# Kernel optimization log

Measured on AMD Instinct MI355X. Metric: run time of the kernel, lower is better.

Reference implementation:

```python
import jax, jax.numpy as jnp
import numpy as np

B, L, H = 8, 512, 768
W = 5          # max_phrase_len
K = 32         # max_phrases
P = 256        # phrase_dim
EPS = 1e-5
NEG = -1e30


def layernorm(x, g, b):
    m = jnp.mean(x, axis=-1, keepdims=True)
    v = jnp.var(x, axis=-1, keepdims=True)
    return (x - m) * jax.lax.rsqrt(v + EPS) * g + b


def setup_inputs() -> dict:
    key = jax.random.key(0)
    ks = jax.random.split(key, 12)
    s = 0.02
    return {
        "hidden": jax.random.normal(ks[0], (B, L, H), dtype=jnp.float32),
        "attention_mask": jnp.ones((B, L), dtype=jnp.int32),
        # span_scorer: Linear(4H->H), LayerNorm(H), ReLU, Linear(H->1)
        "w1": jax.random.normal(ks[1], (4 * H, H), dtype=jnp.float32) * s,
        "b1": jnp.zeros((H,), dtype=jnp.float32),
        "g1": jnp.ones((H,), dtype=jnp.float32),
        "beta1": jnp.zeros((H,), dtype=jnp.float32),
        "w2": jax.random.normal(ks[2], (H, 1), dtype=jnp.float32) * s,
        "b2": jnp.zeros((1,), dtype=jnp.float32),
        # proj: Linear(H->P)
        "wp": jax.random.normal(ks[3], (H, P), dtype=jnp.float32) * s,
        "bp": jnp.zeros((P,), dtype=jnp.float32),
        # attention_gate: Linear(H->H/2), Tanh, Linear(H/2->1)
        "wg1": jax.random.normal(ks[4], (H, H // 2), dtype=jnp.float32) * s,
        "bg1": jnp.zeros((H // 2,), dtype=jnp.float32),
        "wg2": jax.random.normal(ks[5], (H // 2, 1), dtype=jnp.float32) * s,
        "bg2": jnp.zeros((1,), dtype=jnp.float32),
        # out_norm: LayerNorm(P)
        "gout": jnp.ones((P,), dtype=jnp.float32),
        "bout": jnp.zeros((P,), dtype=jnp.float32),
    }


def reference(hidden, attention_mask, w1, b1, g1, beta1, w2, b2,
              wp, bp, wg1, bg1, wg2, bg2, gout, bout):
    mask = attention_mask.astype(bool)  # [B,L]
    # validity of span (i, j=i+w): all tokens i..i+w in mask and i+w < L
    valids = []
    v = mask
    for w in range(W):
        if w > 0:
            shifted = jnp.pad(mask[:, w:], ((0, 0), (0, w)), constant_values=False)
            v = v & shifted
        valids.append(v)
    valid = jnp.stack(valids, axis=2)  # [B,L,W]

    # span means via prefix sums
    prefix = jnp.pad(jnp.cumsum(hidden, axis=1), ((0, 0), (1, 0), (0, 0)))  # [B,L+1,H]
    i_idx = jnp.arange(L)
    j_idx = jnp.minimum(i_idx[:, None] + jnp.arange(W)[None, :], L - 1)  # [L,W]

    start = hidden[:, :, None, :]                                  # [B,L,1,H]
    end = hidden[:, j_idx]                                         # [B,L,W,H]
    span_sum = prefix[:, j_idx + 1] - prefix[:, i_idx][:, :, None, :]
    mean = span_sum / (jnp.arange(W, dtype=hidden.dtype) + 1.0)[None, None, :, None]
    diff = end - start
    start_b = jnp.broadcast_to(start, end.shape)
    feat = jnp.concatenate([start_b, end, mean, diff], axis=-1)    # [B,L,W,4H]

    h = feat @ w1 + b1
    h = jax.nn.relu(layernorm(h, g1, beta1))                       # dropout is eval-mode identity
    score = (h @ w2 + b2)[..., 0]                                  # [B,L,W]
    score = jnp.where(valid, score, NEG)

    flat_scores = score.reshape(B, L * W)
    top_scores, top_idx = jax.lax.top_k(flat_scores, K)            # [B,K]
    phrase_masks = top_scores > NEG / 2

    mean_flat = mean.reshape(B, L * W, H)
    embs = jnp.take_along_axis(mean_flat, top_idx[..., None], axis=1)  # [B,K,H]
    embs = jnp.where(phrase_masks[..., None], embs, 0.0)               # zero-pad features
    phrase_scores = jnp.where(phrase_masks, top_scores, -10.0)

    ti = top_idx // W
    tw = top_idx % W
    spans = jnp.stack([ti, ti + tw], axis=-1)                      # [B,K,2]
    spans = jnp.where(phrase_masks[..., None], spans, 0)

    gate_logits = (jnp.tanh(embs @ wg1 + bg1) @ wg2 + bg2)[..., 0]  # [B,K]
    gate_logits = jnp.where(phrase_masks, gate_logits, -1e9)
    phrase_attention = jax.nn.softmax(gate_logits, axis=-1)

    phrase_embeds = layernorm(embs @ wp + bp, gout, bout)           # [B,K,P]
    return phrase_embeds, phrase_masks, phrase_attention, phrase_scores, spans
```

## Files before the change

### kernel.cpp

```cpp
#include <hip/hip_runtime.h>
#include <float.h>
#include <math.h>

#define B_   8
#define L_   512
#define H_   768
#define W_   5
#define K_   32
#define P_   256
#define EPS_ 1e-5f
#define NEG_ -1e30f

typedef _Float16 half8 __attribute__((ext_vector_type(8)));
typedef _Float16 half4v __attribute__((ext_vector_type(4)));
typedef float floatx4 __attribute__((ext_vector_type(4)));

static const size_t OFF_X   = 0;
static const size_t OFF_AH  = 9437184;
static const size_t OFF_AL  = 11010048;
static const size_t OFF_BH  = 12582912;
static const size_t OFF_BL  = 13467648;
static const size_t OFF_SC  = 14352384;
static const size_t OFF_TS  = 14372864;
static const size_t OFF_TI  = 14373120;
static const size_t OFF_GL  = 14373376;
static const size_t OFF_EMB = 14373632;
static const size_t OFF_Y   = 14570240;

#define A_SCALE 8.0f
#define B_SCALE 64.0f
#define INV_SCALE (1.0f / 512.0f)

__global__ __launch_bounds__(256) void prep_kernel(const float* __restrict__ hid,
                                                   const float* __restrict__ w1,
                                                   _Float16* __restrict__ ah,
                                                   _Float16* __restrict__ al,
                                                   _Float16* __restrict__ bh,
                                                   _Float16* __restrict__ bl) {
    __shared__ float ld[64][65];
    if (blockIdx.x < 3072) {
        int idx = (blockIdx.x * 256 + threadIdx.x) * 4;
        float4 x = *(const float4*)(hid + idx);
        float xs[4] = {x.x * A_SCALE, x.y * A_SCALE, x.z * A_SCALE, x.w * A_SCALE};
        half4v h, l;
#pragma unroll
        for (int i = 0; i < 4; ++i) {
            _Float16 hi = (_Float16)xs[i];
            h[i] = hi;
            l[i] = (_Float16)(xs[i] - (float)hi);
        }
        *(half4v*)(ah + idx) = h;
        *(half4v*)(al + idx) = l;
    } else {
        int bid = blockIdx.x - 3072;
        int n0 = (bid / 12) * 64;
        int k0 = (bid % 12) * 64;
        int t = threadIdx.x;
        int rsel = n0 / 768;
        int c0 = n0 - rsel * 768;
#pragma unroll 4
        for (int r = 0; r < 16; ++r) {
            int idx = r * 256 + t;
            int kk = idx >> 6, nn = idx & 63;
            int k = k0 + kk, c = c0 + nn;
            float v;
            if (rsel == 0)      v = w1[(size_t)k * 768 + c] - w1[(size_t)(2304 + k) * 768 + c];
            else if (rsel == 1) v = w1[(size_t)(768 + k) * 768 + c] + w1[(size_t)(2304 + k) * 768 + c];
            else                v = w1[(size_t)(1536 + k) * 768 + c];
            ld[kk][nn] = v * B_SCALE;
        }
        __syncthreads();
#pragma unroll 4
        for (int r = 0; r < 16; ++r) {
            int idx = r * 256 + t;
            int nn = idx >> 6, kk = idx & 63;
            float v = ld[kk][nn];
            _Float16 h = (_Float16)v;
            _Float16 lo = (_Float16)(v - (float)h);
            size_t o = (size_t)(n0 + nn) * 768 + k0 + kk;
            bh[o] = h;
            bl[o] = lo;
        }
    }
}

typedef const __attribute__((address_space(1))) void* gas_ptr;
typedef __attribute__((address_space(3))) void* las_ptr;
__device__ __forceinline__ void async_ld16(const _Float16* g, _Float16* l) {
    __builtin_amdgcn_global_load_lds((gas_ptr)g, (las_ptr)l, 16, 0, 0);
}

__global__ __launch_bounds__(256) void mfma_gemm_kernel(const _Float16* __restrict__ Ah,
                                                        const _Float16* __restrict__ Al,
                                                        const _Float16* __restrict__ Bh,
                                                        const _Float16* __restrict__ Bl,
                                                        float* __restrict__ C) {
    __shared__ _Float16 sAh[2 * 4096];
    __shared__ _Float16 sAl[2 * 4096];
    __shared__ _Float16 sBh[2 * 2048];
    __shared__ _Float16 sBl[2 * 2048];
    int tid = threadIdx.x;
    int lane = tid & 63;
    int wave = tid >> 6;
    int m0 = blockIdx.x * 128, n0 = blockIdx.y * 64;

    const _Float16* src = (wave == 0) ? Ah : (wave == 1) ? Al : (wave == 2) ? Bh : Bl;
    _Float16* dstb = (wave == 0) ? sAh : (wave == 1) ? sAl : (wave == 2) ? sBh : sBl;
    int psz  = (wave < 2) ? 4096 : 2048;
    int nch  = (wave < 2) ? 8 : 4;
    int row0 = (wave < 2) ? m0 : n0;
    int qg = (lane & 3) ^ ((lane >> 3) & 3);
    const _Float16* gp = src + (size_t)(row0 + (lane >> 2)) * 768 + qg * 8;

    int wr = wave >> 1, wc = wave & 1;
    int off_lane = (lane & 15) * 64 + (((lane >> 4) ^ ((lane >> 1) & 3)) * 16);
    floatx4 acc[4][2];
#pragma unroll
    for (int i = 0; i < 4; ++i)
#pragma unroll
        for (int j = 0; j < 2; ++j)
            acc[i][j] = (floatx4){0.f, 0.f, 0.f, 0.f};

#pragma unroll
    for (int c = 0; c < 8; ++c) {
        if (c < nch) async_ld16(gp + (size_t)c * 16 * 768, dstb + c * 512);
    }

    int parity = 0;
    for (int k0 = 0; k0 < 768; k0 += 32) {
        __syncthreads();
        if (k0 + 32 < 768) {
            _Float16* dst = dstb + (parity ^ 1) * psz;
            const _Float16* g = gp + k0 + 32;
#pragma unroll
            for (int c = 0; c < 8; ++c) {
                if (c < nch) async_ld16(g + (size_t)c * 16 * 768, dst + c * 512);
            }
        }

        const char* bAh = (const char*)sAh + parity * 8192 + wr * 4096 + off_lane;
        const char* bAl = (const char*)sAl + parity * 8192 + wr * 4096 + off_lane;
        const char* bBh = (const char*)sBh + parity * 4096 + wc * 2048 + off_lane;
        const char* bBl = (const char*)sBl + parity * 4096 + wc * 2048 + off_lane;
        half8 a_h[4], a_l[4], b_h[2], b_l[2];
#pragma unroll
        for (int i = 0; i < 4; ++i) {
            a_h[i] = *(const half8*)(bAh + i * 1024);
            a_l[i] = *(const half8*)(bAl + i * 1024);
        }
#pragma unroll
        for (int j = 0; j < 2; ++j) {
            b_h[j] = *(const half8*)(bBh + j * 1024);
            b_l[j] = *(const half8*)(bBl + j * 1024);
        }
#pragma unroll
        for (int i = 0; i < 4; ++i)
#pragma unroll
            for (int j = 0; j < 2; ++j) {
                acc[i][j] = __builtin_amdgcn_mfma_f32_16x16x32_f16(a_h[i], b_h[j], acc[i][j], 0, 0, 0);
                acc[i][j] = __builtin_amdgcn_mfma_f32_16x16x32_f16(a_h[i], b_l[j], acc[i][j], 0, 0, 0);
                acc[i][j] = __builtin_amdgcn_mfma_f32_16x16x32_f16(a_l[i], b_h[j], acc[i][j], 0, 0, 0);
            }
        parity ^= 1;
    }

    int colc = lane & 15, quad = lane >> 4;
#pragma unroll
    for (int i = 0; i < 4; ++i) {
#pragma unroll
        for (int r = 0; r < 4; ++r) {
            int row = m0 + wr * 64 + i * 16 + quad * 4 + r;
            float* Cp = C + (size_t)row * 2304 + n0 + wc * 32 + colc;
#pragma unroll
            for (int j = 0; j < 2; ++j)
                Cp[j * 16] = acc[i][j][r] * INV_SCALE;
        }
    }
}

__global__ __launch_bounds__(256) void score_kernel(const float* __restrict__ X,
                                                    const int* __restrict__ mask,
                                                    const float* __restrict__ b1,
                                                    const float* __restrict__ g1,
                                                    const float* __restrict__ beta1,
                                                    const float* __restrict__ w2,
                                                    const float* __restrict__ b2,
                                                    float* __restrict__ scores) {
    int wave = threadIdx.x >> 6;
    int lane = threadIdx.x & 63;
    int bi = blockIdx.x * 4 + wave;
    int b = bi >> 9, i = bi & 511;

    float4 a[3], b1c[3], g1c[3], btc[3], w2c[3], ss[3], e[3];
    const float4* Xrow = (const float4*)(X + (size_t)bi * 2304);
#pragma unroll
    for (int q = 0; q < 3; ++q) {
        int f = lane + q * 64;
        a[q]   = Xrow[f];
        b1c[q] = ((const float4*)b1)[f];
        g1c[q] = ((const float4*)g1)[f];
        btc[q] = ((const float4*)beta1)[f];
        w2c[q] = ((const float4*)w2)[f];
        ss[q]  = make_float4(0.f, 0.f, 0.f, 0.f);
    }
    float bias2 = b2[0];
    int jcur = i - 1;
    float sc_loc[W_];

    for (int w = 0; w < W_; ++w) {
        int j = min(i + w, 511);
        const float4* Xj = (const float4*)(X + (size_t)(b * 512 + j) * 2304);
        if (j > jcur) {
#pragma unroll
            for (int q = 0; q < 3; ++q) {
                int f = lane + q * 64;
                float4 cc = Xj[384 + f];
                ss[q].x += cc.x; ss[q].y += cc.y; ss[q].z += cc.z; ss[q].w += cc.w;
                e[q] = Xj[192 + f];
            }
            jcur = j;
        }
        float invw = 1.0f / (float)(w + 1);
        float4 h[3];
        float psum = 0.f;
#pragma unroll
        for (int q = 0; q < 3; ++q) {
            h[q].x = a[q].x + e[q].x + ss[q].x * invw + b1c[q].x;
            h[q].y = a[q].y + e[q].y + ss[q].y * invw + b1c[q].y;
            h[q].z = a[q].z + e[q].z + ss[q].z * invw + b1c[q].z;
            h[q].w = a[q].w + e[q].w + ss[q].w * invw + b1c[q].w;
            psum += h[q].x + h[q].y + h[q].z + h[q].w;
        }
#pragma unroll
        for (int m = 1; m < 64; m <<= 1) psum += __shfl_xor(psum, m, 64);
        float mean = psum * (1.f / 768.f);

        float pv = 0.f;
#pragma unroll
        for (int q = 0; q < 3; ++q) {
            float dx = h[q].x - mean, dy = h[q].y - mean, dz = h[q].z - mean, dw = h[q].w - mean;
            pv += dx * dx + dy * dy + dz * dz + dw * dw;
        }
#pragma unroll
        for (int m = 1; m < 64; m <<= 1) pv += __shfl_xor(pv, m, 64);
        float rstd = rsqrtf(pv * (1.f / 768.f) + EPS_);

        float pd = 0.f;
#pragma unroll
        for (int q = 0; q < 3; ++q) {
            float yx = fmaxf((h[q].x - mean) * rstd * g1c[q].x + btc[q].x, 0.f);
            float yy = fmaxf((h[q].y - mean) * rstd * g1c[q].y + btc[q].y, 0.f);
            float yz = fmaxf((h[q].z - mean) * rstd * g1c[q].z + btc[q].z, 0.f);
            float yw = fmaxf((h[q].w - mean) * rstd * g1c[q].w + btc[q].w, 0.f);
            pd += yx * w2c[q].x + yy * w2c[q].y + yz * w2c[q].z + yw * w2c[q].w;
        }
#pragma unroll
        for (int m = 1; m < 64; m <<= 1) pd += __shfl_xor(pd, m, 64);
        sc_loc[w] = pd + bias2;
    }

    if (lane < W_) {
        int w = lane;
        bool ok = (i + w) < 512;
        if (ok) {
            for (int t = 0; t <= w; ++t) ok = ok && (mask[b * 512 + i + t] != 0);
        }
        scores[b * 2560 + i * 5 + w] = ok ? sc_loc[w] : NEG_;
    }
}

__global__ __launch_bounds__(256) void topk_kernel(const float* __restrict__ scores,
                                                   float* __restrict__ tops,
                                                   int* __restrict__ topi,
                                                   float* __restrict__ out_masks,
                                                   float* __restrict__ out_scores,
                                                   float* __restrict__ out_spans) {
    int b = blockIdx.x;
    int tid = threadIdx.x;
    int lane = tid & 63;
    int wv = tid >> 6;
    __shared__ float sc[2560];
    __shared__ float wv_v[4];
    __shared__ int   wv_i[4];
    for (int t = tid; t < 2560; t += 256) sc[t] = scores[b * 2560 + t];
    __syncthreads();

    for (int k = 0; k < K_; ++k) {
        float bv = -FLT_MAX; int bix = 1 << 30;
        for (int t = tid; t < 2560; t += 256) {
            float v = sc[t];
            if (v > bv || (v == bv && t < bix)) { bv = v; bix = t; }
        }
#pragma unroll
        for (int m = 1; m < 64; m <<= 1) {
            float v2 = __shfl_xor(bv, m, 64);
            int   i2 = __shfl_xor(bix, m, 64);
            if (v2 > bv || (v2 == bv && i2 < bix)) { bv = v2; bix = i2; }
        }
        if (lane == 0) { wv_v[wv] = bv; wv_i[wv] = bix; }
        __syncthreads();
        if (tid == 0) {
            float tv = wv_v[0]; int tix = wv_i[0];
            for (int q = 1; q < 4; ++q) {
                if (wv_v[q] > tv || (wv_v[q] == tv && wv_i[q] < tix)) { tv = wv_v[q]; tix = wv_i[q]; }
            }
            tops[b * 32 + k] = tv;
            topi[b * 32 + k] = tix;
            bool m = tv > (NEG_ * 0.5f);
            out_masks[b * 32 + k] = m ? 1.0f : 0.0f;
            out_scores[b * 32 + k] = m ? tv : -10.0f;
            int tI = tix / 5, tw = tix % 5;
            out_spans[(b * 32 + k) * 2 + 0] = m ? (float)tI : 0.0f;
            out_spans[(b * 32 + k) * 2 + 1] = m ? (float)(tI + tw) : 0.0f;
            sc[tix] = -FLT_MAX;
        }
        __syncthreads();
    }
}

__global__ __launch_bounds__(256) void gather_emb_kernel(const float* __restrict__ hidden,
                                                         const float* __restrict__ tops,
                                                         const int* __restrict__ topi,
                                                         float* __restrict__ Embs) {
    int bk = blockIdx.x;
    int b = bk >> 5;
    int tid = threadIdx.x;
    int idx = topi[bk];
    bool valid = tops[bk] > (NEG_ * 0.5f);
    int tI = idx / 5, tw = idx % 5;
    int jend = min(tI + tw, L_ - 1);
    float inv = 1.0f / (float)(tw + 1);
#pragma unroll
    for (int q = 0; q < 3; ++q) {
        int c = tid + q * 256;
        float s = 0.f;
        if (valid) {
            for (int l = tI; l <= jend; ++l) s += hidden[(size_t)(b * 512 + l) * 768 + c];
            s *= inv;
        }
        Embs[(size_t)bk * 768 + c] = s;
    }
}

__global__ __launch_bounds__(256) void phrase_gemm_kernel(const float* __restrict__ Embs,
                                                          const float* __restrict__ wg1,
                                                          const float* __restrict__ bg1,
                                                          const float* __restrict__ wp,
                                                          const float* __restrict__ bp,
                                                          float* __restrict__ Y) {
    __shared__ float As[32][34];
    __shared__ float Bs[32][64];
    int tid = threadIdx.x;
    int m0 = blockIdx.x * 32;
    int cn0 = blockIdx.y * 64;
    const float* Wp; const float* biasp; int ldw;
    if (cn0 < 384) { Wp = wg1 + cn0;        biasp = bg1 + cn0;        ldw = 384; }
    else           { Wp = wp + (cn0 - 384); biasp = bp + (cn0 - 384); ldw = 256; }

    int tx = tid & 15;
    int ty = tid >> 4;
    int ar = tid >> 3, akq = (tid & 7) * 4;
    int bk = tid >> 3, bcq = (tid & 7) * 8;
    float acc[2][4] = {};

    for (int k0 = 0; k0 < 768; k0 += 32) {
        float4 av  = *(const float4*)(Embs + (size_t)(m0 + ar) * 768 + k0 + akq);
        float4 bv0 = *(const float4*)(Wp + (size_t)(k0 + bk) * ldw + bcq);
        float4 bv1 = *(const float4*)(Wp + (size_t)(k0 + bk) * ldw + bcq + 4);
        __syncthreads();
        As[akq + 0][ar] = av.x;
        As[akq + 1][ar] = av.y;
        As[akq + 2][ar] = av.z;
        As[akq + 3][ar] = av.w;
        *(float4*)&Bs[bk][bcq]     = bv0;
        *(float4*)&Bs[bk][bcq + 4] = bv1;
        __syncthreads();
#pragma unroll
        for (int kk = 0; kk < 32; ++kk) {
            float2 a = *(const float2*)&As[kk][ty * 2];
            float4 b = *(const float4*)&Bs[kk][tx * 4];
            acc[0][0] += a.x * b.x; acc[0][1] += a.x * b.y; acc[0][2] += a.x * b.z; acc[0][3] += a.x * b.w;
            acc[1][0] += a.y * b.x; acc[1][1] += a.y * b.y; acc[1][2] += a.y * b.z; acc[1][3] += a.y * b.w;
        }
    }
#pragma unroll
    for (int i = 0; i < 2; ++i) {
        float* Yp = Y + (size_t)(m0 + ty * 2 + i) * 640 + cn0 + tx * 4;
        float4 o = make_float4(acc[i][0] + biasp[tx * 4 + 0], acc[i][1] + biasp[tx * 4 + 1],
                               acc[i][2] + biasp[tx * 4 + 2], acc[i][3] + biasp[tx * 4 + 3]);
        *(float4*)Yp = o;
    }
}

__global__ __launch_bounds__(256) void phrase_post_kernel(const float* __restrict__ Y,
                                                          const float* __restrict__ wg2,
                                                          const float* __restrict__ bg2,
                                                          const float* __restrict__ tops,
                                                          const float* __restrict__ gout,
                                                          const float* __restrict__ bout,
                                                          float* __restrict__ gate,
                                                          float* __restrict__ out_embeds) {
    int wv = threadIdx.x >> 6, lane = threadIdx.x & 63;
    int row = blockIdx.x * 4 + wv;
    const float* Yrow = Y + (size_t)row * 640;

    float s = 0.f;
#pragma unroll
    for (int q = 0; q < 6; ++q) {
        int c = lane + q * 64;
        s += tanhf(Yrow[c]) * wg2[c];
    }
#pragma unroll
    for (int m = 1; m < 64; m <<= 1) s += __shfl_xor(s, m, 64);
    if (lane == 0) {
        bool valid = tops[row] > (NEG_ * 0.5f);
        gate[row] = valid ? (s + bg2[0]) : -1e9f;
    }

    float4 p = *(const float4*)(Yrow + 384 + lane * 4);
    float sm = p.x + p.y + p.z + p.w;
#pragma unroll
    for (int m = 1; m < 64; m <<= 1) sm += __shfl_xor(sm, m, 64);
    float mean = sm * (1.f / 256.f);
    float dx = p.x - mean, dy = p.y - mean, dz = p.z - mean, dw = p.w - mean;
    float v = dx * dx + dy * dy + dz * dz + dw * dw;
#pragma unroll
    for (int m = 1; m < 64; m <<= 1) v += __shfl_xor(v, m, 64);
    float rstd = rsqrtf(v * (1.f / 256.f) + EPS_);
    int c = lane * 4;
    float4 o;
    o.x = dx * rstd * gout[c]     + bout[c];
    o.y = dy * rstd * gout[c + 1] + bout[c + 1];
    o.z = dz * rstd * gout[c + 2] + bout[c + 2];
    o.w = dw * rstd * gout[c + 3] + bout[c + 3];
    *(float4*)(out_embeds + (size_t)row * 256 + c) = o;
}

__global__ void attn_kernel(const float* __restrict__ gate, float* __restrict__ out_attn) {
    int b = threadIdx.x;
    if (b < 8) {
        float mx = -FLT_MAX;
        for (int k = 0; k < 32; ++k) mx = fmaxf(mx, gate[b * 32 + k]);
        float e[32];
        float s = 0.f;
        for (int k = 0; k < 32; ++k) { e[k] = expf(gate[b * 32 + k] - mx); s += e[k]; }
        float inv = 1.f / s;
        for (int k = 0; k < 32; ++k) out_attn[b * 32 + k] = e[k] * inv;
    }
}

extern "C" void kernel_launch(void* const* d_in, const int* in_sizes, int n_in,
                              void* d_out, int out_size, void* d_ws, size_t ws_size,
                              hipStream_t stream) {
    const float* hidden = (const float*)d_in[0];
    const int*   amask  = (const int*)d_in[1];
    const float* w1     = (const float*)d_in[2];
    const float* b1     = (const float*)d_in[3];
    const float* g1     = (const float*)d_in[4];
    const float* beta1  = (const float*)d_in[5];
    const float* w2     = (const float*)d_in[6];
    const float* b2     = (const float*)d_in[7];
    const float* wp     = (const float*)d_in[8];
    const float* bp     = (const float*)d_in[9];
    const float* wg1    = (const float*)d_in[10];
    const float* bg1    = (const float*)d_in[11];
    const float* wg2    = (const float*)d_in[12];
    const float* bg2    = (const float*)d_in[13];
    const float* gout   = (const float*)d_in[14];
    const float* bout   = (const float*)d_in[15];

    float* ws = (float*)d_ws;
    float*     X    = ws + OFF_X;
    _Float16*  ah   = (_Float16*)(ws + OFF_AH);
    _Float16*  al   = (_Float16*)(ws + OFF_AL);
    _Float16*  bh   = (_Float16*)(ws + OFF_BH);
    _Float16*  bl   = (_Float16*)(ws + OFF_BL);
    float*     sc   = ws + OFF_SC;
    float*     ts   = ws + OFF_TS;
    int*       ti   = (int*)(ws + OFF_TI);
    float*     gl   = ws + OFF_GL;
    float*     Embs = ws + OFF_EMB;
    float*     Y    = ws + OFF_Y;

    float* out = (float*)d_out;
    float* out_embeds = out;
    float* out_masks  = out + 65536;
    float* out_attn   = out + 65792;
    float* out_scores = out + 66048;
    float* out_spans  = out + 66304;

    prep_kernel<<<3504, 256, 0, stream>>>(hidden, w1, ah, al, bh, bl);
    mfma_gemm_kernel<<<dim3(32, 36), 256, 0, stream>>>(ah, al, bh, bl, X);
    score_kernel<<<1024, 256, 0, stream>>>(X, amask, b1, g1, beta1, w2, b2, sc);
    topk_kernel<<<8, 256, 0, stream>>>(sc, ts, ti, out_masks, out_scores, out_spans);
    gather_emb_kernel<<<256, 256, 0, stream>>>(hidden, ts, ti, Embs);
    phrase_gemm_kernel<<<dim3(8, 10), 256, 0, stream>>>(Embs, wg1, bg1, wp, bp, Y);
    phrase_post_kernel<<<64, 256, 0, stream>>>(Y, wg2, bg2, ts, gout, bout, gl, out_embeds);
    attn_kernel<<<1, 64, 0, stream>>>(gl, out_attn);
}
```

Before: 276.3 us.

## Rewrite top-k as per-thread sorted lists with packed 64-bit key reduction

Each thread loads its 10 scores and packs each one into a 64-bit key: an order-preserving float encoding in the high bits and an inverted index in the low bits. The thread sorts its keys locally with an odd-even transposition network and keeps only its head key live. Each of the 32 selection rounds then does a single packed max reduction, and only the winning thread advances to its next key. This removes the 10-element shared-memory rescan per round and the separate index comparison. The cost is more register pressure for the sort and two 32-bit shuffles per reduction step.

```diff
diff --git a/kernel.cpp b/kernel.cpp
--- a/kernel.cpp
+++ b/kernel.cpp
@@ -1,6 +1,7 @@
 #include <hip/hip_runtime.h>
 #include <float.h>
 #include <math.h>
+#include <stdint.h>
 
 #define B_   8
 #define L_   512
@@ -269,6 +270,13 @@
     }
 }
 
+__device__ __forceinline__ uint64_t shfl_xor_u64(uint64_t x, int m) {
+    uint32_t lo = (uint32_t)x, hi = (uint32_t)(x >> 32);
+    lo = (uint32_t)__shfl_xor((int)lo, m, 64);
+    hi = (uint32_t)__shfl_xor((int)hi, m, 64);
+    return ((uint64_t)hi << 32) | lo;
+}
+
 __global__ __launch_bounds__(256) void topk_kernel(const float* __restrict__ scores,
                                                    float* __restrict__ tops,
                                                    int* __restrict__ topi,
@@ -279,42 +287,68 @@
     int tid = threadIdx.x;
     int lane = tid & 63;
     int wv = tid >> 6;
-    __shared__ float sc[2560];
-    __shared__ float wv_v[4];
-    __shared__ int   wv_i[4];
-    for (int t = tid; t < 2560; t += 256) sc[t] = scores[b * 2560 + t];
-    __syncthreads();
+    __shared__ uint64_t lists[256 * 9];
+    __shared__ uint64_t wmax[4];
+    __shared__ uint64_t gS;
+
+    uint64_t v[10];
+#pragma unroll
+    for (int q = 0; q < 10; ++q) {
+        int t = q * 256 + tid;
+        float f = scores[b * 2560 + t];
+        uint32_t bits = __float_as_uint(f);
+        uint32_t mk = bits ^ ((bits & 0x80000000u) ? 0xFFFFFFFFu : 0x80000000u);
+        v[q] = ((uint64_t)mk << 32) | (uint64_t)(0xFFFFFFFFu - (uint32_t)t);
+    }
+#pragma unroll
+    for (int p = 0; p < 5; ++p) {
+#pragma unroll
+        for (int i = 0; i < 9; i += 2) {
+            if (v[i] < v[i + 1]) { uint64_t t = v[i]; v[i] = v[i + 1]; v[i + 1] = t; }
+        }
+#pragma unroll
+        for (int i = 1; i < 9; i += 2) {
+            if (v[i] < v[i + 1]) { uint64_t t = v[i]; v[i] = v[i + 1]; v[i + 1] = t; }
+        }
+    }
+#pragma unroll
+    for (int j = 0; j < 9; ++j) lists[tid * 9 + j] = v[j + 1];
+    uint64_t my = v[0];
+    int h = 0;
 
     for (int k = 0; k < K_; ++k) {
-        float bv = -FLT_MAX; int bix = 1 << 30;
-        for (int t = tid; t < 2560; t += 256) {
-            float v = sc[t];
-            if (v > bv || (v == bv && t < bix)) { bv = v; bix = t; }
-        }
-#pragma unroll
-        for (int m = 1; m < 64; m <<= 1) {
-            float v2 = __shfl_xor(bv, m, 64);
-            int   i2 = __shfl_xor(bix, m, 64);
-            if (v2 > bv || (v2 == bv && i2 < bix)) { bv = v2; bix = i2; }
-        }
-        if (lane == 0) { wv_v[wv] = bv; wv_i[wv] = bix; }
+        uint64_t m = my;
+#pragma unroll
+        for (int s = 1; s < 64; s <<= 1) {
+            uint64_t o = shfl_xor_u64(m, s);
+            if (o > m) m = o;
+        }
+        if (lane == 0) wmax[wv] = m;
         __syncthreads();
         if (tid == 0) {
-            float tv = wv_v[0]; int tix = wv_i[0];
-            for (int q = 1; q < 4; ++q) {
-                if (wv_v[q] > tv || (wv_v[q] == tv && wv_i[q] < tix)) { tv = wv_v[q]; tix = wv_i[q]; }
-            }
+            uint64_t g = wmax[0];
+#pragma unroll
+            for (int q = 1; q < 4; ++q) if (wmax[q] > g) g = wmax[q];
+            gS = g;
+            uint32_t mk = (uint32_t)(g >> 32);
+            uint32_t bits = mk ^ ((mk & 0x80000000u) ? 0x80000000u : 0xFFFFFFFFu);
+            float tv = __uint_as_float(bits);
+            int tix = (int)(0xFFFFFFFFu - (uint32_t)(g & 0xFFFFFFFFu));
             tops[b * 32 + k] = tv;
             topi[b * 32 + k] = tix;
-            bool m = tv > (NEG_ * 0.5f);
-            out_masks[b * 32 + k] = m ? 1.0f : 0.0f;
-            out_scores[b * 32 + k] = m ? tv : -10.0f;
+            bool mm = tv > (NEG_ * 0.5f);
+            out_masks[b * 32 + k] = mm ? 1.0f : 0.0f;
+            out_scores[b * 32 + k] = mm ? tv : -10.0f;
             int tI = tix / 5, tw = tix % 5;
-            out_spans[(b * 32 + k) * 2 + 0] = m ? (float)tI : 0.0f;
-            out_spans[(b * 32 + k) * 2 + 1] = m ? (float)(tI + tw) : 0.0f;
-            sc[tix] = -FLT_MAX;
+            out_spans[(b * 32 + k) * 2 + 0] = mm ? (float)tI : 0.0f;
+            out_spans[(b * 32 + k) * 2 + 1] = mm ? (float)(tI + tw) : 0.0f;
         }
         __syncthreads();
+        uint64_t g = gS;
+        if (my == g) {
+            my = (h < 9) ? lists[tid * 9 + h] : 0ull;
+            ++h;
+        }
     }
 }
 
```

Result: faster. 236.3 us (-14.5%).
